# Kernel tuning notes

Measured on AMD Instinct MI355X. Metric: run time of the kernel, lower is better.

Reference implementation:

```python
import jax, jax.numpy as jnp
import numpy as np

D_MODEL, D_HEAD, D_MLP, N_HEADS = 768, 64, 3072, 12
BATCH, SEQ = 1, 4096
LN_EPS = 1e-05
IGNORE = -100000.0


def setup_inputs() -> dict:
    key = jax.random.key(0)
    ks = jax.random.split(key, 8)
    s = 0.02
    return {
        "resid_pre": jax.random.normal(ks[0], (BATCH, SEQ, D_MODEL), jnp.float32),
        "ln1_w": jnp.ones((D_MODEL,), jnp.float32),
        "ln1_b": jnp.zeros((D_MODEL,), jnp.float32),
        "ln2_w": jnp.ones((D_MODEL,), jnp.float32),
        "ln2_b": jnp.zeros((D_MODEL,), jnp.float32),
        "W_Q": jax.random.normal(ks[1], (N_HEADS, D_MODEL, D_HEAD), jnp.float32) * s,
        "W_K": jax.random.normal(ks[2], (N_HEADS, D_MODEL, D_HEAD), jnp.float32) * s,
        "W_V": jax.random.normal(ks[3], (N_HEADS, D_MODEL, D_HEAD), jnp.float32) * s,
        "W_O": jax.random.normal(ks[4], (N_HEADS, D_HEAD, D_MODEL), jnp.float32) * s,
        "b_Q": jnp.zeros((N_HEADS, D_HEAD), jnp.float32),
        "b_K": jnp.zeros((N_HEADS, D_HEAD), jnp.float32),
        "b_V": jnp.zeros((N_HEADS, D_HEAD), jnp.float32),
        "b_O": jnp.zeros((D_MODEL,), jnp.float32),
        "W_in": jax.random.normal(ks[5], (D_MODEL, D_MLP), jnp.float32) * s,
        "b_in": jnp.zeros((D_MLP,), jnp.float32),
        "W_out": jax.random.normal(ks[6], (D_MLP, D_MODEL), jnp.float32) * s,
        "b_out": jnp.zeros((D_MODEL,), jnp.float32),
    }


def _layernorm(x, w, b):
    mean = jnp.mean(x, axis=-1, keepdims=True)
    var = jnp.var(x, axis=-1, keepdims=True)  # unbiased=False
    return (x - mean) * jax.lax.rsqrt(var + LN_EPS) * w + b


def _attention(x, W_Q, W_K, W_V, W_O, b_Q, b_K, b_V, b_O):
    # x: [b, s, d_model]; W_{Q,K,V}: [h, d_model, d_head]
    q = jnp.einsum("bsm,hmd->bshd", x, W_Q) + b_Q
    k = jnp.einsum("bsm,hmd->bshd", x, W_K) + b_K
    v = jnp.einsum("bsm,hmd->bshd", x, W_V) + b_V
    scores = jnp.einsum("bqhd,bkhd->bhqk", q, k) / np.sqrt(D_HEAD).astype(np.float32)
    seq = x.shape[1]
    causal = jnp.tril(jnp.ones((seq, seq), bool))  # True where allowed
    scores = jnp.where(causal, scores, IGNORE)
    pattern = jax.nn.softmax(scores, axis=-1)
    z = jnp.einsum("bkhd,bhqk->bqhd", v, pattern)
    return jnp.einsum("bqhd,hdm->bqm", z, W_O) + b_O


def reference(resid_pre, ln1_w, ln1_b, ln2_w, ln2_b,
              W_Q, W_K, W_V, W_O, b_Q, b_K, b_V, b_O,
              W_in, b_in, W_out, b_out):
    resid_mid = _attention(_layernorm(resid_pre, ln1_w, ln1_b),
                           W_Q, W_K, W_V, W_O, b_Q, b_K, b_V, b_O) + resid_pre
    pre = jnp.einsum("bsm,mf->bsf", _layernorm(resid_mid, ln2_w, ln2_b), W_in) + b_in
    post = jax.nn.gelu(pre, approximate=False)  # torch F.gelu default = exact erf
    mlp_out = jnp.einsum("bsf,fm->bsm", post, W_out) + b_out
    resid_post = mlp_out + resid_mid
    return (resid_post, post)
```

## Files before the change

### kernel.cpp

```cpp
#include <hip/hip_runtime.h>
#include <hip/hip_bf16.h>
#include <math.h>

using bf16 = __hip_bfloat16;
using u16  = unsigned short;
using u32  = unsigned int;
using short8 = __attribute__((ext_vector_type(8))) short;
using f32x4  = __attribute__((ext_vector_type(4))) float;

#define AS1 __attribute__((address_space(1)))
#define AS3 __attribute__((address_space(3)))

__device__ __forceinline__ void gld_lds16(const void* g, void* l) {
  __builtin_amdgcn_global_load_lds((const AS1 u32*)g, (AS3 u32*)l, 16, 0, 0);
}

__device__ __forceinline__ bool probe_f32(const void* p) {
  return *(const u32*)p == 0x3F800000u;
}
__device__ __forceinline__ float ldf(const void* p, size_t i, bool f32) {
  return f32 ? ((const float*)p)[i] : __bfloat162float(((const bf16*)p)[i]);
}
__device__ __forceinline__ void stf(void* p, size_t i, float v, bool f32) {
  if (f32) ((float*)p)[i] = v;
  else     ((bf16*)p)[i] = __float2bfloat16(v);
}
__device__ __forceinline__ u32 cvt_pk_bf16(float lo, float hi) {
  u32 r;
  asm("v_cvt_pk_bf16_f32 %0, %1, %2" : "=v"(r) : "v"(lo), "v"(hi));
  return r;
}

__global__ __launch_bounds__(256) void ln_kernel(const void* __restrict__ x,
    const void* __restrict__ w, const void* __restrict__ b, bf16* __restrict__ out,
    const void* probe, int x_is_f32)
{
  const bool pf = probe_f32(probe);
  const bool xf = x_is_f32 ? true : pf;
  const int row = blockIdx.x, t = threadIdx.x;
  const size_t base = (size_t)row * 768;
  float v[3]; float s1 = 0.f, s2 = 0.f;
#pragma unroll
  for (int i = 0; i < 3; ++i) { float f = ldf(x, base + i*256 + t, xf); v[i] = f; s1 += f; s2 += f*f; }
#pragma unroll
  for (int off = 32; off >= 1; off >>= 1) { s1 += __shfl_xor(s1, off); s2 += __shfl_xor(s2, off); }
  __shared__ float a1[4], a2[4];
  if ((t & 63) == 0) { a1[t>>6] = s1; a2[t>>6] = s2; }
  __syncthreads();
  float S1 = a1[0]+a1[1]+a1[2]+a1[3];
  float S2 = a2[0]+a2[1]+a2[2]+a2[3];
  float mean = S1 * (1.f/768.f);
  float var  = S2 * (1.f/768.f) - mean*mean;
  float rs = rsqrtf(var + 1e-5f);
#pragma unroll
  for (int i = 0; i < 3; ++i) {
    int c = i*256 + t;
    out[base + c] = __float2bfloat16((v[i]-mean)*rs*ldf(w, c, pf) + ldf(b, c, pf));
  }
}

__global__ __launch_bounds__(256) void prep_all(
    const void* W_Q, const void* W_K, const void* W_V, const void* Wo,
    const void* Win, const void* Wout,
    const void* bQ, const void* bK, const void* bV, const void* bO,
    const void* bIn, const void* bOut,
    bf16* __restrict__ qkvT, bf16* __restrict__ WoT, bf16* __restrict__ WinT,
    bf16* __restrict__ WoutT, float* __restrict__ biasA,
    const void* __restrict__ xres, const void* lw, const void* lb,
    bf16* __restrict__ lnout, const void* probe)
{
  const bool pf = probe_f32(probe);
  const int bid = blockIdx.x;
  const int t = threadIdx.x;
  if (bid >= 6939) {
    const int row = bid - 6939;
    const size_t base = (size_t)row * 768;
    float v[3]; float s1 = 0.f, s2 = 0.f;
#pragma unroll
    for (int i = 0; i < 3; ++i) { float f = ldf(xres, base + i*256 + t, pf); v[i] = f; s1 += f; s2 += f*f; }
#pragma unroll
    for (int off = 32; off >= 1; off >>= 1) { s1 += __shfl_xor(s1, off); s2 += __shfl_xor(s2, off); }
    __shared__ float a1[4], a2[4];
    if ((t & 63) == 0) { a1[t>>6] = s1; a2[t>>6] = s2; }
    __syncthreads();
    float S1 = a1[0]+a1[1]+a1[2]+a1[3];
    float S2 = a2[0]+a2[1]+a2[2]+a2[3];
    float mean = S1 * (1.f/768.f);
    float var  = S2 * (1.f/768.f) - mean*mean;
    float rs = rsqrtf(var + 1e-5f);
#pragma unroll
    for (int i = 0; i < 3; ++i) {
      int c = i*256 + t;
      lnout[base + c] = __float2bfloat16((v[i]-mean)*rs*ldf(lw, c, pf) + ldf(lb, c, pf));
    }
    return;
  }
  if (bid >= 6912) {
    int i = (bid - 6912)*256 + t;
    float v;
    if (i < 2304)      v = (i < 768) ? ldf(bQ, i, pf) : (i < 1536 ? ldf(bK, i-768, pf) : ldf(bV, i-1536, pf));
    else if (i < 3072) v = ldf(bO, i-2304, pf);
    else if (i < 6144) v = ldf(bIn, i-3072, pf);
    else               v = ldf(bOut, i-6144, pf);
    biasA[i] = v;
    return;
  }
  const void* src; bf16* dst; int R, C, bx, by; size_t soff = 0;
  if (bid < 1728) {
    int mtx = bid / 576, within = bid % 576;
    int h = within / 48, tt = within % 48;
    by = tt >> 1; bx = tt & 1;
    src = (mtx == 0) ? W_Q : (mtx == 1 ? W_K : W_V);
    soff = (size_t)h * 49152;
    dst = qkvT + ((size_t)mtx*768 + h*64) * 768;
    R = 768; C = 64;
  } else if (bid < 2304) {
    int within = bid - 1728; bx = within % 24; by = within / 24;
    src = Wo; dst = WoT; R = 768; C = 768;
  } else if (bid < 4608) {
    int within = bid - 2304; bx = within % 96; by = within / 96;
    src = Win; dst = WinT; R = 768; C = 3072;
  } else {
    int within = bid - 4608; bx = within % 24; by = within / 24;
    src = Wout; dst = WoutT; R = 3072; C = 768;
  }
  __shared__ bf16 tile[32][33];
  const int bc = bx*32, br = by*32;
  const int tx = t & 31, ty = t >> 5;
#pragma unroll
  for (int i = 0; i < 32; i += 8)
    tile[ty+i][tx] = __float2bfloat16(ldf(src, soff + (size_t)(br+ty+i)*C + bc + tx, pf));
  __syncthreads();
#pragma unroll
  for (int i = 0; i < 32; i += 8)
    dst[(size_t)(bc+ty+i)*R + br + tx] = tile[tx][ty+i];
}

template<int MODE, int BM, int BN, int BK>
__global__ __launch_bounds__(256) void gemm_bt(const bf16* __restrict__ A,
    const bf16* __restrict__ BT, const float* __restrict__ bias,
    const void* __restrict__ res, void* __restrict__ Cout, bf16* __restrict__ aux,
    size_t outOff, const void* probe, int M, int N, int K,
    float* __restrict__ zf, float* __restrict__ sf)
{
  constexpr int MR = BM/32, NR = BN/32;
  constexpr int CH = BK/8;
  __shared__ bf16 Alds[BM*BK];
  __shared__ bf16 Blds[BN*BK];
  const int tid = threadIdx.x;
  const int lane = tid & 63, w = tid >> 6;
  const int l15 = lane & 15, l4 = lane >> 4;

  if (MODE == 0) {
    int bid = blockIdx.y * gridDim.x + blockIdx.x;
    float4 z4 = {0.f, 0.f, 0.f, 0.f};
    float4* zp = (float4*)zf + (size_t)bid*1024;
#pragma unroll
    for (int i = 0; i < 4; ++i) zp[i*256 + tid] = z4;
    if (tid < 16) ((float4*)sf)[bid*16 + tid] = z4;
  }

  const int brow = blockIdx.y * BM, bcol = blockIdx.x * BN;
  const int wr = (w >> 1) * (BM/2), wc = (w & 1) * (BN/2);
  const bf16* Ag = A  + (size_t)brow * K;
  const bf16* Bg = BT + (size_t)bcol * K;
  f32x4 acc[MR][NR];
#pragma unroll
  for (int i = 0; i < MR; ++i)
#pragma unroll
    for (int j = 0; j < NR; ++j) acc[i][j] = 0.f;

  for (int kt = 0; kt < K; kt += BK) {
    if (MODE == 4) {
      const float* Zfp = (const float*)A;
#pragma unroll
      for (int i = 0; i < BM*CH/256; ++i) {
        int id = i*256 + tid, r = id >> 4, cc = id & 15;
        int sw = (r ^ (r >> 3)) & 7;
        const float* srcp = Zfp + (size_t)(brow + r)*768 + kt + cc*8;
        float4 f0 = *(const float4*)srcp;
        float4 f1 = *(const float4*)(srcp + 4);
        float sc = __builtin_amdgcn_rcpf(sf[(size_t)((kt + cc*8) >> 6)*4096 + brow + r]);
        u32 pk[4];
        pk[0] = cvt_pk_bf16(f0.x*sc, f0.y*sc);
        pk[1] = cvt_pk_bf16(f0.z*sc, f0.w*sc);
        pk[2] = cvt_pk_bf16(f1.x*sc, f1.y*sc);
        pk[3] = cvt_pk_bf16(f1.z*sc, f1.w*sc);
        *(uint4*)((char*)Alds + r*(BK*2) + ((cc ^ sw) << 4)) = *(uint4*)pk;
      }
    } else {
#pragma unroll
      for (int i = 0; i < BM*CH/256; ++i) {
        int id = i*256 + tid, r = id / CH, cc = id % CH;
        int sw = (r ^ (r >> 3)) & 7;
        gld_lds16(Ag + (size_t)r*K + kt + ((cc ^ sw) * 8), (char*)Alds + id*16);
      }
    }
#pragma unroll
    for (int i = 0; i < BN*CH/256; ++i) {
      int id = i*256 + tid, r = id / CH, cc = id % CH;
      int sw = (r ^ (r >> 3)) & 7;
      gld_lds16(Bg + (size_t)r*K + kt + ((cc ^ sw) * 8), (char*)Blds + id*16);
    }
    __syncthreads();
#pragma unroll
    for (int kk = 0; kk < BK/32; ++kk) {
      short8 a[MR], b[NR];
#pragma unroll
      for (int mi = 0; mi < MR; ++mi) {
        int row = wr + mi*16 + l15, sw = (row ^ (row >> 3)) & 7;
        a[mi] = *(const short8*)((const char*)Alds + row*(BK*2) + (((kk*4 + l4) ^ sw) << 4));
      }
#pragma unroll
      for (int ni = 0; ni < NR; ++ni) {
        int row = wc + ni*16 + l15, sw = (row ^ (row >> 3)) & 7;
        b[ni] = *(const short8*)((const char*)Blds + row*(BK*2) + (((kk*4 + l4) ^ sw) << 4));
      }
      __builtin_amdgcn_s_setprio(1);
#pragma unroll
      for (int mi = 0; mi < MR; ++mi)
#pragma unroll
        for (int ni = 0; ni < NR; ++ni)
          acc[mi][ni] = __builtin_amdgcn_mfma_f32_16x16x32_bf16(a[mi], b[ni], acc[mi][ni], 0, 0, 0);
      __builtin_amdgcn_s_setprio(0);
    }
    __syncthreads();
  }

  const bool pf = probe_f32(probe);
#pragma unroll
  for (int mi = 0; mi < MR; ++mi) {
#pragma unroll
    for (int r = 0; r < 4; ++r) {
      int row = brow + wr + mi*16 + l4*4 + r;
      size_t rowoff = (size_t)row * N;
#pragma unroll
      for (int ni = 0; ni < NR; ++ni) {
        int col = bcol + wc + ni*16 + l15;
        float v = acc[mi][ni][r] + bias[col];
        if (MODE == 4) v += ldf(res, rowoff + col, pf);
        if (MODE == 3) v += ((const float*)res)[rowoff + col];
        if (MODE == 2) v = 0.5f * v * (1.0f + erff(v * 0.70710678118654752f));
        if (MODE == 0) ((bf16*)Cout)[rowoff + col] = __float2bfloat16(v);
        else if (MODE == 4) ((float*)Cout)[rowoff + col] = v;
        else {
          stf(Cout, outOff + rowoff + col, v, pf);
          if (MODE == 2) aux[rowoff + col] = __float2bfloat16(v);
        }
      }
    }
  }
}

__global__ __launch_bounds__(256) void attn_kernel(const bf16* __restrict__ QKV,
    float* __restrict__ Zf, float* __restrict__ Sf)
{
  __shared__ bf16 Ks[2][4096];
  __shared__ bf16 VTs[2][4096];
  __shared__ bf16 Ps[4][1024];
  const int cid = 159 - blockIdx.x, h = blockIdx.y;
  int qb, c;
  if (cid < 16)      { qb = cid;                    c = 0; }
  else if (cid < 48) { qb = 16 + ((cid-16) >> 1);   c = (cid-16) & 1; }
  else if (cid < 96) { qb = 32 + (cid-48)/3;        c = (cid-48)%3; }
  else               { qb = 48 + ((cid-96) >> 2);   c = (cid-96) & 3; }
  const int t_lo = c*16, t_hi = min(c*16 + 16, qb + 1);

  const int tid = threadIdx.x, lane = tid & 63, w = tid >> 6;
  const int l15 = lane & 15, l4 = lane >> 4;
  const int q0 = qb * 64;

  short8 qf[2];
#pragma unroll
  for (int kk = 0; kk < 2; ++kk)
    qf[kk] = *(const short8*)(QKV + (size_t)(q0 + w*16 + l15)*2304 + h*64 + kk*32 + l4*8);

  int kaddr[2][4], pst[4], pld[2], vwa[8];
#pragma unroll
  for (int kk = 0; kk < 2; ++kk)
#pragma unroll
    for (int ct = 0; ct < 4; ++ct) {
      int krow = ct*16 + l15, sk = (krow ^ (krow >> 3)) & 7;
      kaddr[kk][ct] = krow*128 + (((kk*4 + l4) ^ sk) << 4);
    }
#pragma unroll
  for (int r = 0; r < 4; ++r) {
    int prow = l4*4 + r, sp = (prow ^ (prow >> 3)) & 7;
    pst[r] = prow*128 + (((l15 >> 1) ^ sp) << 4) + (l15 & 1)*8;
  }
#pragma unroll
  for (int kg = 0; kg < 2; ++kg) {
    int sp2 = (l15 ^ (l15 >> 3)) & 7;
    pld[kg] = l15*128 + (((kg*4 + l4) ^ sp2) << 4);
  }
  const int vw = tid >> 3, vd0 = (tid & 7) * 8;
  const int vk0 = (vw >> 1) + (vw & 1) * 32;
#pragma unroll
  for (int d = 0; d < 8; ++d) {
    int row = vd0 + d, srow = (row ^ (row >> 3)) & 7;
    vwa[d] = row*128 + (((vw >> 2) ^ srow) << 4) + (vw & 3)*4;
  }

  const ptrdiff_t STEP = 64*2304;
  int id0 = tid, r0 = id0 >> 3;
  int s0 = (r0 ^ (r0 >> 3)) & 7, c0 = ((id0 & 7) ^ s0) * 8;
  int id1 = 256 + tid, r1 = id1 >> 3;
  int s1 = (r1 ^ (r1 >> 3)) & 7, c1 = ((id1 & 7) ^ s1) * 8;
  const bf16* kgp0 = QKV + (size_t)(t_lo*64 + r0)*2304 + 768 + h*64 + c0;
  const bf16* kgp1 = QKV + (size_t)(t_lo*64 + r1)*2304 + 768 + h*64 + c1;
  const int ksd0 = id0*16, ksd1 = id1*16;
  const bf16* vgp0 = QKV + (size_t)(t_lo*64 + vk0)*2304 + 1536 + h*64 + vd0;
  const bf16* vgp1 = vgp0 + (size_t)16*2304;
  uint4 va, vb, ka, kb;

  ka = *(const uint4*)kgp0;  kgp0 += STEP;
  kb = *(const uint4*)kgp1;  kgp1 += STEP;
  va = *(const uint4*)vgp0;  vgp0 += STEP;
  vb = *(const uint4*)vgp1;  vgp1 += STEP;
  *(uint4*)((char*)Ks[0] + ksd0) = ka;
  *(uint4*)((char*)Ks[0] + ksd1) = kb;
  {
    const u16* pa = (const u16*)&va; const u16* pb = (const u16*)&vb;
#pragma unroll
    for (int d = 0; d < 8; ++d)
      *(u32*)((char*)VTs[0] + vwa[d]) = (u32)pa[d] | ((u32)pb[d] << 16);
  }
  __syncthreads();

  f32x4 o[4]; f32x4 osum;
#pragma unroll
  for (int dt = 0; dt < 4; ++dt) o[dt] = 0.f;
  osum = 0.f;
  short8 ones8;
#pragma unroll
  for (int j = 0; j < 8; ++j) ones8[j] = 0x3F80;

#define ABODY(CUR, NT) {                                                        \
    const int nt_ = (NT);                                                       \
    const bool pref_ = (nt_ + 1 < t_hi);                                        \
    if (pref_) {                                                                \
      ka = *(const uint4*)kgp0;  kgp0 += STEP;                                  \
      kb = *(const uint4*)kgp1;  kgp1 += STEP;                                  \
      va = *(const uint4*)vgp0;  vgp0 += STEP;                                  \
      vb = *(const uint4*)vgp1;  vgp1 += STEP;                                  \
    }                                                                           \
    f32x4 s4[4];                                                                \
    _Pragma("unroll") for (int ct = 0; ct < 4; ++ct) s4[ct] = 0.f;              \
    __builtin_amdgcn_s_setprio(1);                                              \
    _Pragma("unroll") for (int kk = 0; kk < 2; ++kk)                            \
      _Pragma("unroll") for (int ct = 0; ct < 4; ++ct) {                        \
        short8 bk = *(const short8*)((const char*)Ks[0] + kaddr[kk][ct] + (CUR)*8192); \
        s4[ct] = __builtin_amdgcn_mfma_f32_16x16x32_bf16(qf[kk], bk, s4[ct], 0, 0, 0); \
      }                                                                         \
    __builtin_amdgcn_s_setprio(0);                                              \
    const bool diag_ = (nt_ == qb);                                             \
    _Pragma("unroll") for (int r = 0; r < 4; ++r) {                             \
      float p_[4];                                                              \
      _Pragma("unroll") for (int ct = 0; ct < 4; ++ct) {                        \
        float sv = s4[ct][r] * 0.18033688f;                                     \
        if (diag_ && (ct*16 + l15 > w*16 + l4*4 + r)) sv = -30000.0f;           \
        p_[ct] = exp2f(fminf(sv, 43.0f));                                       \
      }                                                                         \
      uint2 pk;                                                                 \
      pk.x = cvt_pk_bf16(p_[0], p_[1]);                                         \
      pk.y = cvt_pk_bf16(p_[2], p_[3]);                                         \
      *(uint2*)((char*)&Ps[w][0] + pst[r]) = pk;                                \
    }                                                                           \
    __builtin_amdgcn_s_setprio(1);                                              \
    _Pragma("unroll") for (int kg = 0; kg < 2; ++kg) {                          \
      short8 ap = *(const short8*)((const char*)&Ps[w][0] + pld[kg]);           \
      _Pragma("unroll") for (int dt = 0; dt < 4; ++dt) {                        \
        short8 bv = *(const short8*)((const char*)VTs[0] + kaddr[kg][dt] + (CUR)*8192); \
        o[dt] = __builtin_amdgcn_mfma_f32_16x16x32_bf16(ap, bv, o[dt], 0, 0, 0); \
      }                                                                         \
      osum = __builtin_amdgcn_mfma_f32_16x16x32_bf16(ap, ones8, osum, 0, 0, 0); \
    }                                                                           \
    __builtin_amdgcn_s_setprio(0);                                              \
    if (pref_) {                                                                \
      *(uint4*)((char*)Ks[0] + ksd0 + ((CUR)^1)*8192) = ka;                     \
      *(uint4*)((char*)Ks[0] + ksd1 + ((CUR)^1)*8192) = kb;                     \
      const u16* pa_ = (const u16*)&va; const u16* pb_ = (const u16*)&vb;       \
      _Pragma("unroll") for (int d = 0; d < 8; ++d)                             \
        *(u32*)((char*)VTs[0] + vwa[d] + ((CUR)^1)*8192) = (u32)pa_[d] | ((u32)pb_[d] << 16); \
    }                                                                           \
    __syncthreads();                                                            \
  }

  const int n = t_hi - t_lo;
  int j2 = 0;
  for (; j2 + 2 <= n; j2 += 2) {
    ABODY(0, t_lo + j2);
    ABODY(1, t_lo + j2 + 1);
  }
  if (j2 < n) ABODY(0, t_lo + j2);
#undef ABODY

  const int qrow0 = q0 + w*16 + l4*4;
#pragma unroll
  for (int r = 0; r < 4; ++r)
    if (l15 == 0) unsafeAtomicAdd(&Sf[(size_t)h*4096 + qrow0 + r], osum[r]);
#pragma unroll
  for (int dt = 0; dt < 4; ++dt)
#pragma unroll
    for (int r = 0; r < 4; ++r)
      unsafeAtomicAdd(&Zf[(size_t)(qrow0 + r)*768 + h*64 + dt*16 + l15], o[dt][r]);
}

extern "C" void kernel_launch(void* const* d_in, const int* in_sizes, int n_in,
                              void* d_out, int out_size, void* d_ws, size_t ws_size,
                              hipStream_t stream)
{
  (void)in_sizes; (void)n_in; (void)out_size; (void)ws_size;
  const void* resid_pre = d_in[0];
  const void* ln1_w = d_in[1];
  const void* ln1_b = d_in[2];
  const void* ln2_w = d_in[3];
  const void* ln2_b = d_in[4];
  const void* W_Q  = d_in[5];
  const void* W_K  = d_in[6];
  const void* W_V  = d_in[7];
  const void* W_O  = d_in[8];
  const void* b_Q  = d_in[9];
  const void* b_K  = d_in[10];
  const void* b_V  = d_in[11];
  const void* b_O  = d_in[12];
  const void* W_in  = d_in[13];
  const void* b_in  = d_in[14];
  const void* W_out = d_in[15];
  const void* b_out = d_in[16];
  const void* probe = ln1_w;

  char* ws = (char*)d_ws;
  bf16*  qkvT  = (bf16*)(ws + 0);
  bf16*  WoT   = (bf16*)(ws + 3538944);
  bf16*  WinT  = (bf16*)(ws + 4718592);
  bf16*  WoutT = (bf16*)(ws + 9437184);
  float* biasA = (float*)(ws + 14155776);
  bf16*  x1    = (bf16*)(ws + 14183424);
  bf16*  QKV   = (bf16*)(ws + 20474880);
  float* Zf    = (float*)(ws + 39349248);
  float* Sf    = (float*)(ws + 51932160);
  float* mid   = (float*)(ws + 20474880);
  bf16*  x2    = (bf16*)(ws + 58223616);
  bf16*  postB = (bf16*)(ws + 33057792);

  prep_all<<<11035, 256, 0, stream>>>(W_Q, W_K, W_V, W_O, W_in, W_out,
      b_Q, b_K, b_V, b_O, b_in, b_out, qkvT, WoT, WinT, WoutT, biasA,
      resid_pre, ln1_w, ln1_b, x1, probe);

  gemm_bt<0,128,96,64><<<dim3(24,32), 256, 0, stream>>>(x1, qkvT, biasA, nullptr, QKV, nullptr, 0, probe, 4096, 2304, 768, Zf, Sf);
  attn_kernel<<<dim3(160,12), 256, 0, stream>>>(QKV, Zf, Sf);
  gemm_bt<4,64,64,128><<<dim3(12,64), 256, 0, stream>>>((const bf16*)Zf, WoT, biasA+2304, resid_pre, mid, nullptr, 0, probe, 4096, 768, 768, nullptr, Sf);
  ln_kernel<<<4096, 256, 0, stream>>>(mid, ln2_w, ln2_b, x2, probe, 1);
  gemm_bt<2,128,128,64><<<dim3(24,32), 256, 0, stream>>>(x2, WinT, biasA+3072, nullptr, d_out, postB, 3145728, probe, 4096, 3072, 768, nullptr, nullptr);
  gemm_bt<3,64,64,128><<<dim3(12,64), 256, 0, stream>>>(postB, WoutT, biasA+6144, mid, d_out, nullptr, 0, probe, 4096, 768, 3072, nullptr, nullptr);
}
```

Before: 227.4 us.

## Double-buffer GEMM LDS tiles and remap workgroups across XCDs for locality

The GEMM kernel now double-buffers its LDS tiles. The next K-tile's global-to-LDS loads are issued before computing on the current tile, and BK is halved so total LDS use stays about the same. A new swizzle handles the BK=32 layout. Workgroup IDs in both the GEMM and attention kernels are remapped so that consecutive logical tiles land on the same XCD, which should improve L2 reuse. The risks are more loop iterations with smaller MFMA batches per barrier and a weaker swizzle for the 32-wide tiles.

```diff
diff --git a/kernel.cpp b/kernel.cpp
--- a/kernel.cpp
+++ b/kernel.cpp
@@ -145,22 +145,26 @@
 {
   constexpr int MR = BM/32, NR = BN/32;
   constexpr int CH = BK/8;
-  __shared__ bf16 Alds[BM*BK];
-  __shared__ bf16 Blds[BN*BK];
+  __shared__ bf16 Alds[2][BM*BK];
+  __shared__ bf16 Blds[2][BN*BK];
   const int tid = threadIdx.x;
   const int lane = tid & 63, w = tid >> 6;
   const int l15 = lane & 15, l4 = lane >> 4;
 
+  const int nwg = gridDim.x * gridDim.y;
+  const int L = blockIdx.x + blockIdx.y * gridDim.x;
+  const int wid = (L & 7) * (nwg >> 3) + (L >> 3);
+  const int bx = wid % gridDim.x, by = wid / gridDim.x;
+
   if (MODE == 0) {
-    int bid = blockIdx.y * gridDim.x + blockIdx.x;
     float4 z4 = {0.f, 0.f, 0.f, 0.f};
-    float4* zp = (float4*)zf + (size_t)bid*1024;
+    float4* zp = (float4*)zf + (size_t)wid*1024;
 #pragma unroll
     for (int i = 0; i < 4; ++i) zp[i*256 + tid] = z4;
-    if (tid < 16) ((float4*)sf)[bid*16 + tid] = z4;
-  }
-
-  const int brow = blockIdx.y * BM, bcol = blockIdx.x * BN;
+    if (tid < 16) ((float4*)sf)[wid*16 + tid] = z4;
+  }
+
+  const int brow = by * BM, bcol = bx * BN;
   const int wr = (w >> 1) * (BM/2), wc = (w & 1) * (BN/2);
   const bf16* Ag = A  + (size_t)brow * K;
   const bf16* Bg = BT + (size_t)bcol * K;
@@ -170,51 +174,66 @@
 #pragma unroll
     for (int j = 0; j < NR; ++j) acc[i][j] = 0.f;
 
-  for (int kt = 0; kt < K; kt += BK) {
+  auto swzf = [](int r) { return BK == 64 ? ((r ^ (r >> 3)) & 7) : ((r >> 1) & 3); };
+
+  auto STAGE = [&](int bb, int kt) {
     if (MODE == 4) {
       const float* Zfp = (const float*)A;
+      const float* sfh = sf + (size_t)(kt >> 6) * 4096 + brow;
 #pragma unroll
       for (int i = 0; i < BM*CH/256; ++i) {
-        int id = i*256 + tid, r = id >> 4, cc = id & 15;
-        int sw = (r ^ (r >> 3)) & 7;
+        int id = i*256 + tid, r = id >> 3, cc = id & 7;
+        int sw = swzf(r);
         const float* srcp = Zfp + (size_t)(brow + r)*768 + kt + cc*8;
         float4 f0 = *(const float4*)srcp;
         float4 f1 = *(const float4*)(srcp + 4);
-        float sc = __builtin_amdgcn_rcpf(sf[(size_t)((kt + cc*8) >> 6)*4096 + brow + r]);
+        float sc = __builtin_amdgcn_rcpf(sfh[r]);
         u32 pk[4];
         pk[0] = cvt_pk_bf16(f0.x*sc, f0.y*sc);
         pk[1] = cvt_pk_bf16(f0.z*sc, f0.w*sc);
         pk[2] = cvt_pk_bf16(f1.x*sc, f1.y*sc);
         pk[3] = cvt_pk_bf16(f1.z*sc, f1.w*sc);
-        *(uint4*)((char*)Alds + r*(BK*2) + ((cc ^ sw) << 4)) = *(uint4*)pk;
+        *(uint4*)((char*)Alds[bb] + r*(BK*2) + ((cc ^ sw) << 4)) = *(uint4*)pk;
       }
     } else {
 #pragma unroll
-      for (int i = 0; i < BM*CH/256; ++i) {
-        int id = i*256 + tid, r = id / CH, cc = id % CH;
-        int sw = (r ^ (r >> 3)) & 7;
-        gld_lds16(Ag + (size_t)r*K + kt + ((cc ^ sw) * 8), (char*)Alds + id*16);
-      }
-    }
-#pragma unroll
-    for (int i = 0; i < BN*CH/256; ++i) {
-      int id = i*256 + tid, r = id / CH, cc = id % CH;
-      int sw = (r ^ (r >> 3)) & 7;
-      gld_lds16(Bg + (size_t)r*K + kt + ((cc ^ sw) * 8), (char*)Blds + id*16);
-    }
-    __syncthreads();
+      for (int i = 0; i < (BM*CH + 255)/256; ++i) {
+        int id = i*256 + tid;
+        if ((BM*CH % 256) == 0 || id < BM*CH) {
+          int r = id / CH, cc = id % CH;
+          gld_lds16(Ag + (size_t)r*K + kt + ((cc ^ swzf(r)) * 8), (char*)Alds[bb] + id*16);
+        }
+      }
+    }
+#pragma unroll
+    for (int i = 0; i < (BN*CH + 255)/256; ++i) {
+      int id = i*256 + tid;
+      if ((BN*CH % 256) == 0 || id < BN*CH) {
+        int r = id / CH, cc = id % CH;
+        gld_lds16(Bg + (size_t)r*K + kt + ((cc ^ swzf(r)) * 8), (char*)Blds[bb] + id*16);
+      }
+    }
+  };
+
+  STAGE(0, 0);
+  __syncthreads();
+
+  const int nIt = K / BK;
+  for (int it = 0; it < nIt; ++it) {
+    const int cur = it & 1;
+    if (it + 1 < nIt) STAGE(cur ^ 1, (it + 1) * BK);
 #pragma unroll
     for (int kk = 0; kk < BK/32; ++kk) {
       short8 a[MR], b[NR];
 #pragma unroll
       for (int mi = 0; mi < MR; ++mi) {
-        int row = wr + mi*16 + l15, sw = (row ^ (row >> 3)) & 7;
-        a[mi] = *(const short8*)((const char*)Alds + row*(BK*2) + (((kk*4 + l4) ^ sw) << 4));
+        int row = wr + mi*16 + l15;
+        a[mi] = *(const short8*)((const char*)Alds[cur] + row*(BK*2) + (((kk*4 + l4) ^ swzf(row)) << 4));
       }
 #pragma unroll
       for (int ni = 0; ni < NR; ++ni) {
-        int row = wc + ni*16 + l15, sw = (row ^ (row >> 3)) & 7;
-        b[ni] = *(const short8*)((const char*)Blds + row*(BK*2) + (((kk*4 + l4) ^ sw) << 4));
+        int row = wc + ni*16 + l15;
+        b[ni] = *(const short8*)((const char*)Blds[cur] + row*(BK*2) + (((kk*4 + l4) ^ swzf(row)) << 4));
       }
       __builtin_amdgcn_s_setprio(1);
 #pragma unroll
@@ -258,7 +277,10 @@
   __shared__ bf16 Ks[2][4096];
   __shared__ bf16 VTs[2][4096];
   __shared__ bf16 Ps[4][1024];
-  const int cid = 159 - blockIdx.x, h = blockIdx.y;
+  const int L = blockIdx.x + blockIdx.y * 160;
+  const int wid = (L & 7) * 240 + (L >> 3);
+  const int h = wid / 160;
+  const int cid = 159 - (wid % 160);
   int qb, c;
   if (cid < 16)      { qb = cid;                    c = 0; }
   else if (cid < 48) { qb = 16 + ((cid-16) >> 1);   c = (cid-16) & 1; }
@@ -448,10 +470,10 @@
       b_Q, b_K, b_V, b_O, b_in, b_out, qkvT, WoT, WinT, WoutT, biasA,
       resid_pre, ln1_w, ln1_b, x1, probe);
 
-  gemm_bt<0,128,96,64><<<dim3(24,32), 256, 0, stream>>>(x1, qkvT, biasA, nullptr, QKV, nullptr, 0, probe, 4096, 2304, 768, Zf, Sf);
+  gemm_bt<0,128,96,32><<<dim3(24,32), 256, 0, stream>>>(x1, qkvT, biasA, nullptr, QKV, nullptr, 0, probe, 4096, 2304, 768, Zf, Sf);
   attn_kernel<<<dim3(160,12), 256, 0, stream>>>(QKV, Zf, Sf);
-  gemm_bt<4,64,64,128><<<dim3(12,64), 256, 0, stream>>>((const bf16*)Zf, WoT, biasA+2304, resid_pre, mid, nullptr, 0, probe, 4096, 768, 768, nullptr, Sf);
+  gemm_bt<4,64,64,64><<<dim3(12,64), 256, 0, stream>>>((const bf16*)Zf, WoT, biasA+2304, resid_pre, mid, nullptr, 0, probe, 4096, 768, 768, nullptr, Sf);
   ln_kernel<<<4096, 256, 0, stream>>>(mid, ln2_w, ln2_b, x2, probe, 1);
-  gemm_bt<2,128,128,64><<<dim3(24,32), 256, 0, stream>>>(x2, WinT, biasA+3072, nullptr, d_out, postB, 3145728, probe, 4096, 3072, 768, nullptr, nullptr);
-  gemm_bt<3,64,64,128><<<dim3(12,64), 256, 0, stream>>>(postB, WoutT, biasA+6144, mid, d_out, nullptr, 0, probe, 4096, 768, 3072, nullptr, nullptr);
-}
+  gemm_bt<2,128,128,32><<<dim3(24,32), 256, 0, stream>>>(x2, WinT, biasA+3072, nullptr, d_out, postB, 3145728, probe, 4096, 3072, 768, nullptr, nullptr);
+  gemm_bt<3,64,64,64><<<dim3(12,64), 256, 0, stream>>>(postB, WoutT, biasA+6144, mid, d_out, nullptr, 0, probe, 4096, 768, 3072, nullptr, nullptr);
+}
```

New measurement: 223.8 us (median of 3 runs). No clear change (-1.6%).
